# Performance work log

Hardware: AMD Instinct MI355X
Metric: run time of the kernel (lower is better)

The kernel has to match this reference:

```python
import jax, jax.numpy as jnp
import numpy as np

EPS = 1e-6

def _rms_norm(x, w):
    # RMSNorm over last dim (head_dim)
    var = jnp.mean(jnp.square(x), axis=-1, keepdims=True)
    return x * jax.lax.rsqrt(var + EPS) * w

def _apply_rope(x, cos, sin):
    # x: [b, s, h, d]; cos/sin: [s, d]. Interleaved (real, imag) pairs as in
    # diffusers apply_rotary_emb (use_real_unbind_dim=-1) used by Flux.
    xr = x[..., 0::2]
    xi = x[..., 1::2]
    rotated = jnp.stack([-xi, xr], axis=-1).reshape(x.shape)
    cs = cos[None, :, None, :]
    sn = sin[None, :, None, :]
    return x * cs + rotated * sn

def setup_inputs() -> dict:
    key = jax.random.key(0)
    ks = jax.random.split(key, 10)
    b, s, dim, h, hd = 1, 2048, 3072, 24, 128
    inner = h * hd
    scale = 1.0 / np.sqrt(dim)
    x = jax.random.normal(ks[0], (b, s, dim), dtype=jnp.float32)
    # rope tables: proper cos/sin of log-spaced frequencies
    pos = jnp.arange(s, dtype=jnp.float32)[:, None]
    freqs = 1.0 / (10000.0 ** (jnp.arange(0, hd, 2, dtype=jnp.float32) / hd))
    angles = pos * freqs[None, :]                      # [s, hd/2]
    angles = jnp.repeat(angles, 2, axis=-1)            # [s, hd] interleaved pairs
    rope_cos = jnp.cos(angles)
    rope_sin = jnp.sin(angles)
    Wq = jax.random.normal(ks[1], (dim, inner), dtype=jnp.float32) * scale
    Wk = jax.random.normal(ks[2], (dim, inner), dtype=jnp.float32) * scale
    Wv = jax.random.normal(ks[3], (dim, inner), dtype=jnp.float32) * scale
    bq = jax.random.normal(ks[4], (inner,), dtype=jnp.float32) * 0.01
    bk = jax.random.normal(ks[5], (inner,), dtype=jnp.float32) * 0.01
    bv = jax.random.normal(ks[6], (inner,), dtype=jnp.float32) * 0.01
    gq = jnp.ones((hd,), dtype=jnp.float32)
    gk = jnp.ones((hd,), dtype=jnp.float32)
    return {"x": x, "rope_cos": rope_cos, "rope_sin": rope_sin,
            "Wq": Wq, "bq": bq, "Wk": Wk, "bk": bk, "Wv": Wv, "bv": bv,
            "gq": gq, "gk": gk}

def reference(x, rope_cos, rope_sin, Wq, bq, Wk, bk, Wv, bv, gq, gk):
    b, s, _ = x.shape
    h, hd = 24, 128
    q = (x @ Wq + bq).reshape(b, s, h, hd)
    k = (x @ Wk + bk).reshape(b, s, h, hd)
    v = (x @ Wv + bv).reshape(b, s, h, hd)
    q = _apply_rope(_rms_norm(q, gq), rope_cos, rope_sin)
    k = _apply_rope(_rms_norm(k, gk), rope_cos, rope_sin)
    scale = 1.0 / jnp.sqrt(jnp.asarray(hd, dtype=q.dtype))
    scores = jnp.einsum('bshd,bthd->bhst', q, k) * scale
    attn = jax.nn.softmax(scores, axis=-1)
    out = jnp.einsum('bhst,bthd->bshd', attn, v)
    return out.reshape(b, s, h * hd)
```

## Files before the change

### kernel.cpp

```cpp
#include <hip/hip_runtime.h>
#include <hip/hip_bf16.h>

typedef __attribute__((ext_vector_type(8))) short short8;
typedef __attribute__((ext_vector_type(4))) float f32x4;
typedef __attribute__((ext_vector_type(16))) float f32x16;

#define SEQ 2048
#define DIM 3072
#define NHEAD 24
#define HDIM 128
#define SCALE_Q 0.12751744f

__device__ __forceinline__ unsigned short f2bf(float f) {
  unsigned int b = __float_as_uint(f);
  b += 0x7fffu + ((b >> 16) & 1u);
  return (unsigned short)(b >> 16);
}
__device__ __forceinline__ float bf2f(unsigned short u) {
  return __uint_as_float(((unsigned int)u) << 16);
}
__device__ __forceinline__ unsigned int pkbf(float a, float b) {
  __hip_bfloat162 h = __float22bfloat162_rn(make_float2(a, b));
  return *(unsigned int*)&h;
}

__device__ __forceinline__ void async16(const void* g, void* l) {
  __builtin_amdgcn_global_load_lds(
      (const __attribute__((address_space(1))) unsigned int*)g,
      (__attribute__((address_space(3))) unsigned int*)l, 16, 0, 0);
}

__global__ void k_cvt_x(const float* __restrict__ x, unsigned short* __restrict__ xb) {
  int idx = (blockIdx.x * 256 + threadIdx.x) * 8;
  float4 a = *(const float4*)(x + idx);
  float4 b = *(const float4*)(x + idx + 4);
  short8 o;
  o[0] = (short)f2bf(a.x); o[1] = (short)f2bf(a.y);
  o[2] = (short)f2bf(a.z); o[3] = (short)f2bf(a.w);
  o[4] = (short)f2bf(b.x); o[5] = (short)f2bf(b.y);
  o[6] = (short)f2bf(b.z); o[7] = (short)f2bf(b.w);
  *(short8*)(xb + idx) = o;
}

__device__ __forceinline__ void transpose_tile(const float* __restrict__ w,
                                               unsigned short* __restrict__ wt,
                                               int n0, int k0, int outRowBase, int t) {
  __shared__ unsigned short tile[64][68];
  int c4 = (t & 15) * 4;
  int r0 = t >> 4;
#pragma unroll
  for (int j = 0; j < 4; ++j) {
    int r = r0 + 16 * j;
    float4 v = *(const float4*)(w + (size_t)(k0 + r) * DIM + n0 + c4);
    ushort4 u;
    u.x = f2bf(v.x); u.y = f2bf(v.y); u.z = f2bf(v.z); u.w = f2bf(v.w);
    *(ushort4*)&tile[r][c4] = u;
  }
  __syncthreads();
#pragma unroll
  for (int j = 0; j < 4; ++j) {
    int nn = r0 + 16 * j;
    ushort4 u;
    u.x = tile[c4 + 0][nn]; u.y = tile[c4 + 1][nn];
    u.z = tile[c4 + 2][nn]; u.w = tile[c4 + 3][nn];
    *(ushort4*)(wt + (size_t)(outRowBase + n0 + nn) * DIM + k0 + c4) = u;
  }
}

__global__ __launch_bounds__(256) void k_transpose(const float* __restrict__ w,
                                                   unsigned short* __restrict__ wt) {
  transpose_tile(w, wt, blockIdx.x * 64, blockIdx.y * 64, 0, threadIdx.x);
}

__global__ __launch_bounds__(256) void k_transpose3(const float* __restrict__ w0,
                                                    const float* __restrict__ w1,
                                                    const float* __restrict__ w2,
                                                    unsigned short* __restrict__ wt) {
  const float* w = blockIdx.z == 0 ? w0 : (blockIdx.z == 1 ? w1 : w2);
  transpose_tile(w, wt, blockIdx.x * 64, blockIdx.y * 64, blockIdx.z * DIM, threadIdx.x);
}

__device__ __forceinline__ void gemm_tile(const unsigned short* __restrict__ xb,
                                          const unsigned short* __restrict__ wt,
                                          int bm, int bn, int t, f32x4 (&acc)[4][4],
                                          unsigned short* As, unsigned short* Bs) {
  int l = t & 63, w = t >> 6;
  int wr = w >> 1, wc = w & 1;
  int lr = l & 15, kc = l >> 4;
  const char* aB = (const char*)xb;
  const char* bB = (const char*)wt;
  char* asmB = (char*)As;
  char* bsmB = (char*)Bs;
  int sw = (lr & 7) << 4;

  for (int k0 = 0; k0 < DIM; k0 += 64) {
#pragma unroll
    for (int i = 0; i < 4; ++i) {
      int off = (t + 256 * i) * 16;
      int row = off >> 7;
      int cb = off & 127;
      int scb = cb ^ ((row & 7) << 4);
      async16(aB + ((size_t)(bm * 128 + row) * DIM + k0) * 2 + scb, asmB + off);
      async16(bB + ((size_t)(bn * 128 + row) * DIM + k0) * 2 + scb, bsmB + off);
    }
    __syncthreads();
#pragma unroll
    for (int kk = 0; kk < 2; ++kk) {
      short8 af[4], bf[4];
#pragma unroll
      for (int m = 0; m < 4; ++m)
        af[m] = *(const short8*)(asmB + (wr * 64 + m * 16 + lr) * 128 +
                                 ((kk * 64 + kc * 16) ^ sw));
#pragma unroll
      for (int n = 0; n < 4; ++n)
        bf[n] = *(const short8*)(bsmB + (wc * 64 + n * 16 + lr) * 128 +
                                 ((kk * 64 + kc * 16) ^ sw));
#pragma unroll
      for (int m = 0; m < 4; ++m)
#pragma unroll
        for (int n = 0; n < 4; ++n)
          acc[m][n] = __builtin_amdgcn_mfma_f32_16x16x32_bf16(af[m], bf[n], acc[m][n], 0, 0, 0);
    }
    __syncthreads();
  }
}

__global__ __launch_bounds__(256) void k_gemm(const unsigned short* __restrict__ xb,
                                              const unsigned short* __restrict__ wt,
                                              const float* __restrict__ bias,
                                              unsigned short* __restrict__ out,
                                              int vmode) {
  __shared__ unsigned short As[128 * 64];
  __shared__ unsigned short Bs[128 * 64];
  int t = threadIdx.x;
  int fid = blockIdx.x;
  int logical = (fid & 7) * 48 + (fid >> 3);
  int bm = logical & 15, bn = logical >> 4;

  f32x4 acc[4][4];
#pragma unroll
  for (int m = 0; m < 4; ++m)
#pragma unroll
    for (int n = 0; n < 4; ++n) acc[m][n] = (f32x4){0.f, 0.f, 0.f, 0.f};

  gemm_tile(xb, wt, bm, bn, t, acc, As, Bs);

  int l = t & 63, w = t >> 6;
  int wr = w >> 1, wc = w & 1;
  int lr = l & 15, lq = l >> 4;
  if (vmode) {
#pragma unroll
    for (int m = 0; m < 4; ++m)
#pragma unroll
      for (int n = 0; n < 4; ++n) {
        int gcol = bn * 128 + wc * 64 + n * 16 + lr;
        float bv = bias[gcol];
        int grow = bm * 128 + wr * 64 + m * 16 + lq * 4;
        ushort4 u;
        u.x = f2bf(acc[m][n][0] + bv);
        u.y = f2bf(acc[m][n][1] + bv);
        u.z = f2bf(acc[m][n][2] + bv);
        u.w = f2bf(acc[m][n][3] + bv);
        *(ushort4*)(out + (size_t)gcol * SEQ + grow) = u;
      }
  } else {
#pragma unroll
    for (int m = 0; m < 4; ++m)
#pragma unroll
      for (int n = 0; n < 4; ++n) {
        int gcol = bn * 128 + wc * 64 + n * 16 + lr;
        float bv = bias[gcol];
#pragma unroll
        for (int i = 0; i < 4; ++i) {
          int grow = bm * 128 + wr * 64 + m * 16 + lq * 4 + i;
          out[(size_t)grow * DIM + gcol] = f2bf(acc[m][n][i] + bv);
        }
      }
  }
}

__global__ __launch_bounds__(256, 4) void k_gemm3(
    const unsigned short* __restrict__ xb, const unsigned short* __restrict__ wt,
    const float* __restrict__ bq, const float* __restrict__ bk,
    const float* __restrict__ bv, const float* __restrict__ rope_cos,
    const float* __restrict__ rope_sin, const float* __restrict__ gq,
    const float* __restrict__ gk, unsigned short* __restrict__ qb,
    unsigned short* __restrict__ kb, unsigned short* __restrict__ vtb) {
  __shared__ unsigned short As[128 * 64];
  __shared__ unsigned short Bs[128 * 64];
  __shared__ float ssum[2][128];
  int t = threadIdx.x;
  int fid = blockIdx.x;
  int xcd = fid & 7, li = fid >> 3;
  int c = li / 36, r = li % 36;
  int bnl9 = r >> 2, bmi = r & 3;
  int bm = c * 4 + bmi;
  int bn = xcd * 9 + bnl9;

  f32x4 acc[4][4];
#pragma unroll
  for (int m = 0; m < 4; ++m)
#pragma unroll
    for (int n = 0; n < 4; ++n) acc[m][n] = (f32x4){0.f, 0.f, 0.f, 0.f};

  gemm_tile(xb, wt, bm, bn, t, acc, As, Bs);

  int l = t & 63, w = t >> 6;
  int wr = w >> 1, wc = w & 1;
  int lr = l & 15, lq = l >> 4;

  int region = bn >= 48 ? 2 : (bn >= 24 ? 1 : 0);
  int bnl = bn - region * 24;
  const float* bias = region == 0 ? bq : (region == 1 ? bk : bv);

  if (region == 2) {
#pragma unroll
    for (int m = 0; m < 4; ++m)
#pragma unroll
      for (int n = 0; n < 4; ++n) {
        int gcol = bnl * 128 + wc * 64 + n * 16 + lr;
        float bv_ = bias[gcol];
        int grow = bm * 128 + wr * 64 + m * 16 + lq * 4;
        ushort4 u;
        u.x = f2bf(acc[m][n][0] + bv_);
        u.y = f2bf(acc[m][n][1] + bv_);
        u.z = f2bf(acc[m][n][2] + bv_);
        u.w = f2bf(acc[m][n][3] + bv_);
        *(ushort4*)(vtb + (size_t)gcol * SEQ + grow) = u;
      }
  } else {
    unsigned short* outp = region == 0 ? qb : kb;
    const float* g = region == 0 ? gq : gk;
    float scale = region == 0 ? SCALE_Q : 1.0f;

    float gv[4], bvv[4];
#pragma unroll
    for (int n = 0; n < 4; ++n) {
      int cl = wc * 64 + n * 16 + lr;
      gv[n] = g[cl];
      bvv[n] = bias[bnl * 128 + cl];
    }
#pragma unroll
    for (int m = 0; m < 4; ++m)
#pragma unroll
      for (int n = 0; n < 4; ++n)
#pragma unroll
        for (int i = 0; i < 4; ++i) acc[m][n][i] += bvv[n];

#pragma unroll
    for (int m = 0; m < 4; ++m)
#pragma unroll
      for (int i = 0; i < 4; ++i) {
        float ss = acc[m][0][i] * acc[m][0][i] + acc[m][1][i] * acc[m][1][i] +
                   acc[m][2][i] * acc[m][2][i] + acc[m][3][i] * acc[m][3][i];
        ss += __shfl_xor(ss, 1);
        ss += __shfl_xor(ss, 2);
        ss += __shfl_xor(ss, 4);
        ss += __shfl_xor(ss, 8);
        if (lr == m * 4 + i) ssum[wc][wr * 64 + m * 16 + lq * 4 + i] = ss;
      }
    __syncthreads();

#pragma unroll
    for (int m = 0; m < 4; ++m)
#pragma unroll
      for (int i = 0; i < 4; ++i) {
        int rl = wr * 64 + m * 16 + lq * 4 + i;
        float rn = rsqrtf((ssum[0][rl] + ssum[1][rl]) * (1.0f / 128.0f) + 1e-6f);
        int s_idx = bm * 128 + rl;
        const float* cr = rope_cos + (size_t)s_idx * HDIM;
        const float* sr = rope_sin + (size_t)s_idx * HDIM;
        unsigned short* orow = outp + (size_t)s_idx * DIM + bnl * 128;
#pragma unroll
        for (int n = 0; n < 4; ++n) {
          int cl = wc * 64 + n * 16 + lr;
          float xn = acc[m][n][i] * rn * gv[n];
          float pr = __shfl_xor(xn, 1);
          float cv = cr[cl], sv = sr[cl];
          float o = (lr & 1) ? fmaf(xn, cv, pr * sv) : fmaf(xn, cv, -pr * sv);
          orow[cl] = f2bf(o * scale);
        }
      }
  }
}

__global__ void k_normrope(unsigned short* __restrict__ qk, const float* __restrict__ cosb,
                           const float* __restrict__ sinb, const float* __restrict__ g,
                           float scale) {
  int t = threadIdx.x;
  int w = t >> 6, l = t & 63;
  int row = blockIdx.x * 4 + w;
  int s_idx = row / NHEAD, head = row % NHEAD;
  size_t base = (size_t)s_idx * DIM + head * HDIM;
  unsigned int pair = *(const unsigned int*)(qk + base + 2 * l);
  float x0 = bf2f((unsigned short)(pair & 0xffffu));
  float x1 = bf2f((unsigned short)(pair >> 16));
  float ss = x0 * x0 + x1 * x1;
#pragma unroll
  for (int off = 1; off < 64; off <<= 1) ss += __shfl_xor(ss, off);
  float r = rsqrtf(ss * (1.0f / 128.0f) + 1e-6f);
  float g0 = g[2 * l], g1 = g[2 * l + 1];
  float c0 = cosb[s_idx * HDIM + 2 * l], c1 = cosb[s_idx * HDIM + 2 * l + 1];
  float s0 = sinb[s_idx * HDIM + 2 * l], s1 = sinb[s_idx * HDIM + 2 * l + 1];
  float xn0 = x0 * r * g0, xn1 = x1 * r * g1;
  float o0 = (xn0 * c0 - xn1 * s0) * scale;
  float o1 = (xn1 * c1 + xn0 * s1) * scale;
  unsigned int po = (unsigned int)f2bf(o0) | ((unsigned int)f2bf(o1) << 16);
  *(unsigned int*)(qk + base + 2 * l) = po;
}

__global__ __launch_bounds__(128, 2) void k_attn(const unsigned short* __restrict__ q,
                                                 const unsigned short* __restrict__ k,
                                                 const unsigned short* __restrict__ vt,
                                                 float* __restrict__ out) {
  __shared__ unsigned short Ksm[64 * 128];
  __shared__ unsigned short Vtsm[128 * 64];
  int t = threadIdx.x;
  int w = t >> 6, l = t & 63;
  int q32 = l & 31, hi = l >> 5;
  int hi4 = hi * 4;
  int fid = blockIdx.x;
  int logical = (fid & 7) * 96 + (fid >> 3);
  int qt = logical & 31, h = logical >> 5;
  int q0w = qt * 64 + w * 32;

  const char* kbase = (const char*)k + (size_t)h * HDIM * 2;
  const char* vbase = (const char*)vt + (size_t)h * HDIM * SEQ * 2;

  int koff[8], voff[8];
#pragma unroll
  for (int i = 0; i < 8; ++i) {
    int off = (t + 128 * i) * 16;
    int krow = off >> 8, kcb = off & 255;
    koff[i] = krow * (DIM * 2) + (kcb ^ ((krow & 15) << 4));
    int vrow = off >> 7, vcb = off & 127;
    voff[i] = vrow * (SEQ * 2) + (vcb ^ ((vrow & 7) << 4));
  }

  short8 qf[8];
  {
    const unsigned short* qrow = q + (size_t)(q0w + q32) * DIM + h * HDIM;
#pragma unroll
    for (int ks = 0; ks < 8; ++ks) qf[ks] = *(const short8*)(qrow + ks * 16 + hi * 8);
  }

  f32x16 o0 = {0.f,0.f,0.f,0.f,0.f,0.f,0.f,0.f,0.f,0.f,0.f,0.f,0.f,0.f,0.f,0.f};
  f32x16 o1 = o0, o2 = o0, o3 = o0;
  float m_ = -1e30f, lsum = 0.f;
  int ksw = (q32 & 15) << 4;
  int vsw = (q32 & 7) << 4;

  union U8 { short8 s8; unsigned int u[4]; };

  for (int kt = 0; kt < 32; ++kt) {
    const char* kt_k = kbase + (size_t)kt * (64 * DIM * 2);
    const char* kt_v = vbase + kt * 128;
#pragma unroll
    for (int i = 0; i < 8; ++i) {
      int dst = (t + 128 * i) * 16;
      async16(kt_k + koff[i], (char*)Ksm + dst);
      async16(kt_v + voff[i], (char*)Vtsm + dst);
    }
    __syncthreads();

    f32x16 st0 = {0.f,0.f,0.f,0.f,0.f,0.f,0.f,0.f,0.f,0.f,0.f,0.f,0.f,0.f,0.f,0.f};
    f32x16 st1 = st0;
    {
      const char* kr0 = (const char*)Ksm + q32 * 256;
      const char* kr1 = (const char*)Ksm + (32 + q32) * 256;
      __builtin_amdgcn_s_setprio(1);
#pragma unroll
      for (int ks = 0; ks < 8; ++ks) {
        int cb = (ks * 32 + hi * 16) ^ ksw;
        short8 kf0 = *(const short8*)(kr0 + cb);
        short8 kf1 = *(const short8*)(kr1 + cb);
        st0 = __builtin_amdgcn_mfma_f32_32x32x16_bf16(kf0, qf[ks], st0, 0, 0, 0);
        st1 = __builtin_amdgcn_mfma_f32_32x32x16_bf16(kf1, qf[ks], st1, 0, 0, 0);
      }
      __builtin_amdgcn_s_setprio(0);
    }

    float mx = fmaxf(st0[0], st1[0]);
#pragma unroll
    for (int r = 1; r < 16; ++r) mx = fmaxf(mx, fmaxf(st0[r], st1[r]));
    mx = fmaxf(mx, __shfl_xor(mx, 32));

    if (__any(mx > m_ + 10.0f)) {
      float mn = fmaxf(m_, mx);
      float corr = exp2f(m_ - mn);
      m_ = mn;
      lsum *= corr;
#pragma unroll
      for (int r = 0; r < 16; ++r) {
        float cr = __shfl(corr, (r & 3) + 8 * (r >> 2) + hi4);
        o0[r] *= cr; o1[r] *= cr; o2[r] *= cr; o3[r] *= cr;
      }
    }

#pragma unroll
    for (int r = 0; r < 16; ++r) {
      st0[r] = exp2f(st0[r] - m_);
      st1[r] = exp2f(st1[r] - m_);
    }
    {
      float sm = st0[0] + st1[0];
#pragma unroll
      for (int r = 1; r < 16; ++r) sm += st0[r] + st1[r];
      sm += __shfl_xor(sm, 32);
      lsum += sm;
    }

    U8 pa[4];
#pragma unroll
    for (int b = 0; b < 4; ++b) {
      unsigned int a0, a1, a2, a3;
      if (b < 2) {
        int r0 = (b & 1) * 8;
        a0 = pkbf(st0[r0 + 0], st0[r0 + 1]);
        a1 = pkbf(st0[r0 + 2], st0[r0 + 3]);
        a2 = pkbf(st0[r0 + 4], st0[r0 + 5]);
        a3 = pkbf(st0[r0 + 6], st0[r0 + 7]);
      } else {
        int r0 = (b & 1) * 8;
        a0 = pkbf(st1[r0 + 0], st1[r0 + 1]);
        a1 = pkbf(st1[r0 + 2], st1[r0 + 3]);
        a2 = pkbf(st1[r0 + 4], st1[r0 + 5]);
        a3 = pkbf(st1[r0 + 6], st1[r0 + 7]);
      }
      asm volatile("v_permlane32_swap_b32 %0, %1" : "+v"(a0), "+v"(a2));
      asm volatile("v_permlane32_swap_b32 %0, %1" : "+v"(a1), "+v"(a3));
      pa[b].u[0] = a0; pa[b].u[1] = a1; pa[b].u[2] = a2; pa[b].u[3] = a3;
    }

    __builtin_amdgcn_s_setprio(1);
#pragma unroll
    for (int ks = 0; ks < 4; ++ks) {
      int cb = (ks * 32 + hi * 16) ^ vsw;
      short8 vf0 = *(const short8*)((const char*)Vtsm + (0 * 32 + q32) * 128 + cb);
      short8 vf1 = *(const short8*)((const char*)Vtsm + (1 * 32 + q32) * 128 + cb);
      short8 vf2 = *(const short8*)((const char*)Vtsm + (2 * 32 + q32) * 128 + cb);
      short8 vf3 = *(const short8*)((const char*)Vtsm + (3 * 32 + q32) * 128 + cb);
      o0 = __builtin_amdgcn_mfma_f32_32x32x16_bf16(pa[ks].s8, vf0, o0, 0, 0, 0);
      o1 = __builtin_amdgcn_mfma_f32_32x32x16_bf16(pa[ks].s8, vf1, o1, 0, 0, 0);
      o2 = __builtin_amdgcn_mfma_f32_32x32x16_bf16(pa[ks].s8, vf2, o2, 0, 0, 0);
      o3 = __builtin_amdgcn_mfma_f32_32x32x16_bf16(pa[ks].s8, vf3, o3, 0, 0, 0);
    }
    __builtin_amdgcn_s_setprio(0);

    __syncthreads();
  }

  float inv = 1.0f / lsum;
#pragma unroll
  for (int r = 0; r < 16; ++r) {
    float fr = __shfl(inv, (r & 3) + 8 * (r >> 2) + hi4);
    int grow = q0w + (r & 3) + 8 * (r >> 2) + hi4;
    float* orow = out + (size_t)grow * DIM + h * HDIM + q32;
    orow[0]  = o0[r] * fr;
    orow[32] = o1[r] * fr;
    orow[64] = o2[r] * fr;
    orow[96] = o3[r] * fr;
  }
}

extern "C" void kernel_launch(void* const* d_in, const int* in_sizes, int n_in,
                              void* d_out, int out_size, void* d_ws, size_t ws_size,
                              hipStream_t stream) {
  const float* x = (const float*)d_in[0];
  const float* rope_cos = (const float*)d_in[1];
  const float* rope_sin = (const float*)d_in[2];
  const float* Wq = (const float*)d_in[3];
  const float* bq = (const float*)d_in[4];
  const float* Wk = (const float*)d_in[5];
  const float* bk = (const float*)d_in[6];
  const float* Wv = (const float*)d_in[7];
  const float* bv = (const float*)d_in[8];
  const float* gq = (const float*)d_in[9];
  const float* gk = (const float*)d_in[10];
  float* out = (float*)d_out;

  const size_t slab = (size_t)SEQ * DIM;
  const size_t wt9elems = (size_t)3 * DIM * DIM;
  const size_t need = (4 * slab + wt9elems) * 2;

  if (ws_size >= need) {
    unsigned short* xb = (unsigned short*)d_ws;
    unsigned short* wt9 = xb + slab;
    unsigned short* qb = wt9 + wt9elems;
    unsigned short* kb = qb + slab;
    unsigned short* vtb = kb + slab;

    k_cvt_x<<<3072, 256, 0, stream>>>(x, xb);
    k_transpose3<<<dim3(DIM / 64, DIM / 64, 3), 256, 0, stream>>>(Wq, Wk, Wv, wt9);
    k_gemm3<<<1152, 256, 0, stream>>>(xb, wt9, bq, bk, bv, rope_cos, rope_sin, gq, gk,
                                      qb, kb, vtb);
    k_attn<<<768, 128, 0, stream>>>(qb, kb, vtb, out);
  } else {
    unsigned short* xb = (unsigned short*)d_ws;
    unsigned short* wt = xb + slab;
    unsigned short* qb = wt + (size_t)DIM * DIM;
    unsigned short* kb = qb + slab;
    unsigned short* vtb = kb + slab;

    k_cvt_x<<<3072, 256, 0, stream>>>(x, xb);
    dim3 tg(DIM / 64, DIM / 64);
    k_transpose<<<tg, 256, 0, stream>>>(Wq, wt);
    k_gemm<<<384, 256, 0, stream>>>(xb, wt, bq, qb, 0);
    k_transpose<<<tg, 256, 0, stream>>>(Wk, wt);
    k_gemm<<<384, 256, 0, stream>>>(xb, wt, bk, kb, 0);
    k_transpose<<<tg, 256, 0, stream>>>(Wv, wt);
    k_gemm<<<384, 256, 0, stream>>>(xb, wt, bv, vtb, 1);
    k_normrope<<<SEQ * NHEAD / 4, 256, 0, stream>>>(qb, rope_cos, rope_sin, gq, SCALE_Q);
    k_normrope<<<SEQ * NHEAD / 4, 256, 0, stream>>>(kb, rope_cos, rope_sin, gk, 1.0f);
    k_attn<<<768, 128, 0, stream>>>(qb, kb, vtb, out);
  }
}
```

Before: 286.8 us.

## Enlarge fused QKV GEMM tile to 256x128 with inline MFMA loop

```diff
diff --git a/kernel.cpp b/kernel.cpp
--- a/kernel.cpp
+++ b/kernel.cpp
@@ -179,48 +179,90 @@
   }
 }
 
-__global__ __launch_bounds__(256, 4) void k_gemm3(
+__global__ __launch_bounds__(256, 2) void k_gemm3(
     const unsigned short* __restrict__ xb, const unsigned short* __restrict__ wt,
     const float* __restrict__ bq, const float* __restrict__ bk,
     const float* __restrict__ bv, const float* __restrict__ rope_cos,
     const float* __restrict__ rope_sin, const float* __restrict__ gq,
     const float* __restrict__ gk, unsigned short* __restrict__ qb,
     unsigned short* __restrict__ kb, unsigned short* __restrict__ vtb) {
-  __shared__ unsigned short As[128 * 64];
+  __shared__ unsigned short As[256 * 64];
   __shared__ unsigned short Bs[128 * 64];
-  __shared__ float ssum[2][128];
+  __shared__ float ssum[2][256];
   int t = threadIdx.x;
   int fid = blockIdx.x;
   int xcd = fid & 7, li = fid >> 3;
-  int c = li / 36, r = li % 36;
-  int bnl9 = r >> 2, bmi = r & 3;
-  int bm = c * 4 + bmi;
+  int c = li / 18, r = li % 18;
+  int bnl9 = r >> 1, bmi = r & 1;
+  int bm = c * 2 + bmi;
   int bn = xcd * 9 + bnl9;
-
-  f32x4 acc[4][4];
-#pragma unroll
-  for (int m = 0; m < 4; ++m)
-#pragma unroll
-    for (int n = 0; n < 4; ++n) acc[m][n] = (f32x4){0.f, 0.f, 0.f, 0.f};
-
-  gemm_tile(xb, wt, bm, bn, t, acc, As, Bs);
 
   int l = t & 63, w = t >> 6;
   int wr = w >> 1, wc = w & 1;
-  int lr = l & 15, lq = l >> 4;
-
+  int lr = l & 15, kc = l >> 4;
+  int sw = (lr & 7) << 4;
+
+  f32x4 acc[8][4];
+#pragma unroll
+  for (int m = 0; m < 8; ++m)
+#pragma unroll
+    for (int n = 0; n < 4; ++n) acc[m][n] = (f32x4){0.f, 0.f, 0.f, 0.f};
+
+  const char* aB = (const char*)xb;
+  const char* bB = (const char*)wt;
+  char* asmB = (char*)As;
+  char* bsmB = (char*)Bs;
+
+  for (int k0 = 0; k0 < DIM; k0 += 64) {
+#pragma unroll
+    for (int i = 0; i < 8; ++i) {
+      int off = (t + 256 * i) * 16;
+      int row = off >> 7;
+      int cb = off & 127;
+      int scb = cb ^ ((row & 7) << 4);
+      async16(aB + ((size_t)(bm * 256 + row) * DIM + k0) * 2 + scb, asmB + off);
+    }
+#pragma unroll
+    for (int i = 0; i < 4; ++i) {
+      int off = (t + 256 * i) * 16;
+      int row = off >> 7;
+      int cb = off & 127;
+      int scb = cb ^ ((row & 7) << 4);
+      async16(bB + ((size_t)(bn * 128 + row) * DIM + k0) * 2 + scb, bsmB + off);
+    }
+    __syncthreads();
+#pragma unroll
+    for (int kk = 0; kk < 2; ++kk) {
+      short8 af[8], bf[4];
+      int kb_ = (kk * 64 + kc * 16) ^ sw;
+#pragma unroll
+      for (int m = 0; m < 8; ++m)
+        af[m] = *(const short8*)(asmB + (wr * 128 + m * 16 + lr) * 128 + kb_);
+#pragma unroll
+      for (int n = 0; n < 4; ++n)
+        bf[n] = *(const short8*)(bsmB + (wc * 64 + n * 16 + lr) * 128 + kb_);
+#pragma unroll
+      for (int m = 0; m < 8; ++m)
+#pragma unroll
+        for (int n = 0; n < 4; ++n)
+          acc[m][n] = __builtin_amdgcn_mfma_f32_16x16x32_bf16(af[m], bf[n], acc[m][n], 0, 0, 0);
+    }
+    __syncthreads();
+  }
+
+  int lq = l >> 4;
   int region = bn >= 48 ? 2 : (bn >= 24 ? 1 : 0);
   int bnl = bn - region * 24;
   const float* bias = region == 0 ? bq : (region == 1 ? bk : bv);
 
   if (region == 2) {
 #pragma unroll
-    for (int m = 0; m < 4; ++m)
+    for (int m = 0; m < 8; ++m)
 #pragma unroll
       for (int n = 0; n < 4; ++n) {
         int gcol = bnl * 128 + wc * 64 + n * 16 + lr;
         float bv_ = bias[gcol];
-        int grow = bm * 128 + wr * 64 + m * 16 + lq * 4;
+        int grow = bm * 256 + wr * 128 + m * 16 + lq * 4;
         ushort4 u;
         u.x = f2bf(acc[m][n][0] + bv_);
         u.y = f2bf(acc[m][n][1] + bv_);
@@ -241,14 +283,14 @@
       bvv[n] = bias[bnl * 128 + cl];
     }
 #pragma unroll
-    for (int m = 0; m < 4; ++m)
+    for (int m = 0; m < 8; ++m)
 #pragma unroll
       for (int n = 0; n < 4; ++n)
 #pragma unroll
         for (int i = 0; i < 4; ++i) acc[m][n][i] += bvv[n];
 
 #pragma unroll
-    for (int m = 0; m < 4; ++m)
+    for (int m = 0; m < 8; ++m)
 #pragma unroll
       for (int i = 0; i < 4; ++i) {
         float ss = acc[m][0][i] * acc[m][0][i] + acc[m][1][i] * acc[m][1][i] +
@@ -257,17 +299,17 @@
         ss += __shfl_xor(ss, 2);
         ss += __shfl_xor(ss, 4);
         ss += __shfl_xor(ss, 8);
-        if (lr == m * 4 + i) ssum[wc][wr * 64 + m * 16 + lq * 4 + i] = ss;
-      }
-    __syncthreads();
-
-#pragma unroll
-    for (int m = 0; m < 4; ++m)
+        if (lr == ((m * 4 + i) & 15)) ssum[wc][wr * 128 + m * 16 + lq * 4 + i] = ss;
+      }
+    __syncthreads();
+
+#pragma unroll
+    for (int m = 0; m < 8; ++m)
 #pragma unroll
       for (int i = 0; i < 4; ++i) {
-        int rl = wr * 64 + m * 16 + lq * 4 + i;
+        int rl = wr * 128 + m * 16 + lq * 4 + i;
         float rn = rsqrtf((ssum[0][rl] + ssum[1][rl]) * (1.0f / 128.0f) + 1e-6f);
-        int s_idx = bm * 128 + rl;
+        int s_idx = bm * 256 + rl;
         const float* cr = rope_cos + (size_t)s_idx * HDIM;
         const float* sr = rope_sin + (size_t)s_idx * HDIM;
         unsigned short* orow = outp + (size_t)s_idx * DIM + bnl * 128;
@@ -492,8 +534,8 @@
 
     k_cvt_x<<<3072, 256, 0, stream>>>(x, xb);
     k_transpose3<<<dim3(DIM / 64, DIM / 64, 3), 256, 0, stream>>>(Wq, Wk, Wv, wt9);
-    k_gemm3<<<1152, 256, 0, stream>>>(xb, wt9, bq, bk, bv, rope_cos, rope_sin, gq, gk,
-                                      qb, kb, vtb);
+    k_gemm3<<<576, 256, 0, stream>>>(xb, wt9, bq, bk, bv, rope_cos, rope_sin, gq, gk,
+                                     qb, kb, vtb);
     k_attn<<<768, 128, 0, stream>>>(qb, kb, vtb, out);
   } else {
     unsigned short* xb = (unsigned short*)d_ws;
```

Measured after the change: 312.3 us. 8.9% more time.

## Split KV loop across two wave pairs per block and merge softmax partials

Applied to the files above, without the earlier changes.

```diff
diff --git a/kernel.cpp b/kernel.cpp
--- a/kernel.cpp
+++ b/kernel.cpp
@@ -309,28 +309,30 @@
   *(unsigned int*)(qk + base + 2 * l) = po;
 }
 
-__global__ __launch_bounds__(128, 2) void k_attn(const unsigned short* __restrict__ q,
+__global__ __launch_bounds__(256, 2) void k_attn(const unsigned short* __restrict__ q,
                                                  const unsigned short* __restrict__ k,
                                                  const unsigned short* __restrict__ vt,
                                                  float* __restrict__ out) {
-  __shared__ unsigned short Ksm[64 * 128];
-  __shared__ unsigned short Vtsm[128 * 64];
+  __shared__ unsigned short Ksm[2][64 * 128];
+  __shared__ unsigned short Vtsm[2][128 * 64];
   int t = threadIdx.x;
   int w = t >> 6, l = t & 63;
+  int qhalf = w & 1, par = w >> 1;
   int q32 = l & 31, hi = l >> 5;
   int hi4 = hi * 4;
   int fid = blockIdx.x;
   int logical = (fid & 7) * 96 + (fid >> 3);
   int qt = logical & 31, h = logical >> 5;
-  int q0w = qt * 64 + w * 32;
+  int q0w = qt * 64 + qhalf * 32;
 
   const char* kbase = (const char*)k + (size_t)h * HDIM * 2;
   const char* vbase = (const char*)vt + (size_t)h * HDIM * SEQ * 2;
 
-  int koff[8], voff[8];
-#pragma unroll
-  for (int i = 0; i < 8; ++i) {
-    int off = (t + 128 * i) * 16;
+  int koff[4], voff[4], dst[4];
+#pragma unroll
+  for (int i = 0; i < 4; ++i) {
+    int off = (t + 256 * i) * 16;
+    dst[i] = off;
     int krow = off >> 8, kcb = off & 255;
     koff[i] = krow * (DIM * 2) + (kcb ^ ((krow & 15) << 4));
     int vrow = off >> 7, vcb = off & 127;
@@ -352,22 +354,25 @@
 
   union U8 { short8 s8; unsigned int u[4]; };
 
-  for (int kt = 0; kt < 32; ++kt) {
-    const char* kt_k = kbase + (size_t)kt * (64 * DIM * 2);
-    const char* kt_v = vbase + kt * 128;
-#pragma unroll
-    for (int i = 0; i < 8; ++i) {
-      int dst = (t + 128 * i) * 16;
-      async16(kt_k + koff[i], (char*)Ksm + dst);
-      async16(kt_v + voff[i], (char*)Vtsm + dst);
+  for (int t2 = 0; t2 < 16; ++t2) {
+    int kt0 = t2 * 2;
+#pragma unroll
+    for (int p = 0; p < 2; ++p) {
+      const char* kt_k = kbase + (size_t)(kt0 + p) * (64 * DIM * 2);
+      const char* kt_v = vbase + (kt0 + p) * 128;
+#pragma unroll
+      for (int i = 0; i < 4; ++i) {
+        async16(kt_k + koff[i], (char*)Ksm[p] + dst[i]);
+        async16(kt_v + voff[i], (char*)Vtsm[p] + dst[i]);
+      }
     }
     __syncthreads();
 
     f32x16 st0 = {0.f,0.f,0.f,0.f,0.f,0.f,0.f,0.f,0.f,0.f,0.f,0.f,0.f,0.f,0.f,0.f};
     f32x16 st1 = st0;
     {
-      const char* kr0 = (const char*)Ksm + q32 * 256;
-      const char* kr1 = (const char*)Ksm + (32 + q32) * 256;
+      const char* kr0 = (const char*)Ksm[par] + q32 * 256;
+      const char* kr1 = (const char*)Ksm[par] + (32 + q32) * 256;
       __builtin_amdgcn_s_setprio(1);
 #pragma unroll
       for (int ks = 0; ks < 8; ++ks) {
@@ -436,10 +441,11 @@
 #pragma unroll
     for (int ks = 0; ks < 4; ++ks) {
       int cb = (ks * 32 + hi * 16) ^ vsw;
-      short8 vf0 = *(const short8*)((const char*)Vtsm + (0 * 32 + q32) * 128 + cb);
-      short8 vf1 = *(const short8*)((const char*)Vtsm + (1 * 32 + q32) * 128 + cb);
-      short8 vf2 = *(const short8*)((const char*)Vtsm + (2 * 32 + q32) * 128 + cb);
-      short8 vf3 = *(const short8*)((const char*)Vtsm + (3 * 32 + q32) * 128 + cb);
+      const char* Vp = (const char*)Vtsm[par];
+      short8 vf0 = *(const short8*)(Vp + (0 * 32 + q32) * 128 + cb);
+      short8 vf1 = *(const short8*)(Vp + (1 * 32 + q32) * 128 + cb);
+      short8 vf2 = *(const short8*)(Vp + (2 * 32 + q32) * 128 + cb);
+      short8 vf3 = *(const short8*)(Vp + (3 * 32 + q32) * 128 + cb);
       o0 = __builtin_amdgcn_mfma_f32_32x32x16_bf16(pa[ks].s8, vf0, o0, 0, 0, 0);
       o1 = __builtin_amdgcn_mfma_f32_32x32x16_bf16(pa[ks].s8, vf1, o1, 0, 0, 0);
       o2 = __builtin_amdgcn_mfma_f32_32x32x16_bf16(pa[ks].s8, vf2, o2, 0, 0, 0);
@@ -450,16 +456,40 @@
     __syncthreads();
   }
 
-  float inv = 1.0f / lsum;
-#pragma unroll
-  for (int r = 0; r < 16; ++r) {
-    float fr = __shfl(inv, (r & 3) + 8 * (r >> 2) + hi4);
-    int grow = q0w + (r & 3) + 8 * (r >> 2) + hi4;
-    float* orow = out + (size_t)grow * DIM + h * HDIM + q32;
-    orow[0]  = o0[r] * fr;
-    orow[32] = o1[r] * fr;
-    orow[64] = o2[r] * fr;
-    orow[96] = o3[r] * fr;
+  float* mbase = (float*)(&Ksm[0][0]) + qhalf * 4224;
+  float* oB = mbase;
+  float* mB = mbase + 4096;
+  float* lB = mbase + 4128;
+  if (par == 1) {
+#pragma unroll
+    for (int r = 0; r < 16; ++r) {
+      oB[r * 64 + l]        = o0[r];
+      oB[(16 + r) * 64 + l] = o1[r];
+      oB[(32 + r) * 64 + l] = o2[r];
+      oB[(48 + r) * 64 + l] = o3[r];
+    }
+    if (l < 32) { mB[l] = m_; lB[l] = lsum; }
+  }
+  __syncthreads();
+  if (par == 0) {
+    float mBv = mB[q32];
+    float lBv = lB[q32];
+    float mN = fmaxf(m_, mBv);
+    float cA = exp2f(m_ - mN), cB = exp2f(mBv - mN);
+    float inv = 1.0f / (lsum * cA + lBv * cB);
+    float fA = cA * inv, fB = cB * inv;
+#pragma unroll
+    for (int r = 0; r < 16; ++r) {
+      int crow = (r & 3) + 8 * (r >> 2) + hi4;
+      float sA = __shfl(fA, crow);
+      float sB = __shfl(fB, crow);
+      int grow = q0w + crow;
+      float* orow = out + (size_t)grow * DIM + h * HDIM + q32;
+      orow[0]  = o0[r] * sA + oB[r * 64 + l] * sB;
+      orow[32] = o1[r] * sA + oB[(16 + r) * 64 + l] * sB;
+      orow[64] = o2[r] * sA + oB[(32 + r) * 64 + l] * sB;
+      orow[96] = o3[r] * sA + oB[(48 + r) * 64 + l] * sB;
+    }
   }
 }
 
@@ -494,7 +524,7 @@
     k_transpose3<<<dim3(DIM / 64, DIM / 64, 3), 256, 0, stream>>>(Wq, Wk, Wv, wt9);
     k_gemm3<<<1152, 256, 0, stream>>>(xb, wt9, bq, bk, bv, rope_cos, rope_sin, gq, gk,
                                       qb, kb, vtb);
-    k_attn<<<768, 128, 0, stream>>>(qb, kb, vtb, out);
+    k_attn<<<768, 256, 0, stream>>>(qb, kb, vtb, out);
   } else {
     unsigned short* xb = (unsigned short*)d_ws;
     unsigned short* wt = xb + slab;
@@ -512,6 +542,6 @@
     k_gemm<<<384, 256, 0, stream>>>(xb, wt, bv, vtb, 1);
     k_normrope<<<SEQ * NHEAD / 4, 256, 0, stream>>>(qb, rope_cos, rope_sin, gq, SCALE_Q);
     k_normrope<<<SEQ * NHEAD / 4, 256, 0, stream>>>(kb, rope_cos, rope_sin, gk, 1.0f);
-    k_attn<<<768, 128, 0, stream>>>(qb, kb, vtb, out);
-  }
-}
+    k_attn<<<768, 256, 0, stream>>>(qb, kb, vtb, out);
+  }
+}
```

Measured after the change: 285.2 us. About the same (-0.6%).

## Double-buffer K/V tiles in attention and widen blocks to four waves

Applied to the files above, without the earlier changes.

```diff
diff --git a/kernel.cpp b/kernel.cpp
--- a/kernel.cpp
+++ b/kernel.cpp
@@ -309,28 +309,29 @@
   *(unsigned int*)(qk + base + 2 * l) = po;
 }
 
-__global__ __launch_bounds__(128, 2) void k_attn(const unsigned short* __restrict__ q,
+__global__ __launch_bounds__(256, 2) void k_attn(const unsigned short* __restrict__ q,
                                                  const unsigned short* __restrict__ k,
                                                  const unsigned short* __restrict__ vt,
                                                  float* __restrict__ out) {
-  __shared__ unsigned short Ksm[64 * 128];
-  __shared__ unsigned short Vtsm[128 * 64];
+  __shared__ unsigned short Ksm[2][64 * 128];
+  __shared__ unsigned short Vtsm[2][128 * 64];
   int t = threadIdx.x;
   int w = t >> 6, l = t & 63;
   int q32 = l & 31, hi = l >> 5;
   int hi4 = hi * 4;
   int fid = blockIdx.x;
-  int logical = (fid & 7) * 96 + (fid >> 3);
-  int qt = logical & 31, h = logical >> 5;
-  int q0w = qt * 64 + w * 32;
+  int logical = (fid & 7) * 48 + (fid >> 3);
+  int qt = logical & 15, h = logical >> 4;
+  int q0w = qt * 128 + w * 32;
 
   const char* kbase = (const char*)k + (size_t)h * HDIM * 2;
   const char* vbase = (const char*)vt + (size_t)h * HDIM * SEQ * 2;
 
-  int koff[8], voff[8];
-#pragma unroll
-  for (int i = 0; i < 8; ++i) {
-    int off = (t + 128 * i) * 16;
+  int koff[4], voff[4], dst[4];
+#pragma unroll
+  for (int i = 0; i < 4; ++i) {
+    int off = (t + 256 * i) * 16;
+    dst[i] = off;
     int krow = off >> 8, kcb = off & 255;
     koff[i] = krow * (DIM * 2) + (kcb ^ ((krow & 15) << 4));
     int vrow = off >> 7, vcb = off & 127;
@@ -352,22 +353,30 @@
 
   union U8 { short8 s8; unsigned int u[4]; };
 
+#pragma unroll
+  for (int i = 0; i < 4; ++i) {
+    async16(kbase + koff[i], (char*)Ksm[0] + dst[i]);
+    async16(vbase + voff[i], (char*)Vtsm[0] + dst[i]);
+  }
+  __syncthreads();
+
   for (int kt = 0; kt < 32; ++kt) {
-    const char* kt_k = kbase + (size_t)kt * (64 * DIM * 2);
-    const char* kt_v = vbase + kt * 128;
-#pragma unroll
-    for (int i = 0; i < 8; ++i) {
-      int dst = (t + 128 * i) * 16;
-      async16(kt_k + koff[i], (char*)Ksm + dst);
-      async16(kt_v + voff[i], (char*)Vtsm + dst);
-    }
-    __syncthreads();
+    int cur = kt & 1;
+    if (kt < 31) {
+      const char* kt_k = kbase + (size_t)(kt + 1) * (64 * DIM * 2);
+      const char* kt_v = vbase + (kt + 1) * 128;
+#pragma unroll
+      for (int i = 0; i < 4; ++i) {
+        async16(kt_k + koff[i], (char*)Ksm[cur ^ 1] + dst[i]);
+        async16(kt_v + voff[i], (char*)Vtsm[cur ^ 1] + dst[i]);
+      }
+    }
 
     f32x16 st0 = {0.f,0.f,0.f,0.f,0.f,0.f,0.f,0.f,0.f,0.f,0.f,0.f,0.f,0.f,0.f,0.f};
     f32x16 st1 = st0;
     {
-      const char* kr0 = (const char*)Ksm + q32 * 256;
-      const char* kr1 = (const char*)Ksm + (32 + q32) * 256;
+      const char* kr0 = (const char*)Ksm[cur] + q32 * 256;
+      const char* kr1 = (const char*)Ksm[cur] + (32 + q32) * 256;
       __builtin_amdgcn_s_setprio(1);
 #pragma unroll
       for (int ks = 0; ks < 8; ++ks) {
@@ -436,10 +445,11 @@
 #pragma unroll
     for (int ks = 0; ks < 4; ++ks) {
       int cb = (ks * 32 + hi * 16) ^ vsw;
-      short8 vf0 = *(const short8*)((const char*)Vtsm + (0 * 32 + q32) * 128 + cb);
-      short8 vf1 = *(const short8*)((const char*)Vtsm + (1 * 32 + q32) * 128 + cb);
-      short8 vf2 = *(const short8*)((const char*)Vtsm + (2 * 32 + q32) * 128 + cb);
-      short8 vf3 = *(const short8*)((const char*)Vtsm + (3 * 32 + q32) * 128 + cb);
+      const char* Vp = (const char*)Vtsm[cur];
+      short8 vf0 = *(const short8*)(Vp + (0 * 32 + q32) * 128 + cb);
+      short8 vf1 = *(const short8*)(Vp + (1 * 32 + q32) * 128 + cb);
+      short8 vf2 = *(const short8*)(Vp + (2 * 32 + q32) * 128 + cb);
+      short8 vf3 = *(const short8*)(Vp + (3 * 32 + q32) * 128 + cb);
       o0 = __builtin_amdgcn_mfma_f32_32x32x16_bf16(pa[ks].s8, vf0, o0, 0, 0, 0);
       o1 = __builtin_amdgcn_mfma_f32_32x32x16_bf16(pa[ks].s8, vf1, o1, 0, 0, 0);
       o2 = __builtin_amdgcn_mfma_f32_32x32x16_bf16(pa[ks].s8, vf2, o2, 0, 0, 0);
@@ -494,7 +504,7 @@
     k_transpose3<<<dim3(DIM / 64, DIM / 64, 3), 256, 0, stream>>>(Wq, Wk, Wv, wt9);
     k_gemm3<<<1152, 256, 0, stream>>>(xb, wt9, bq, bk, bv, rope_cos, rope_sin, gq, gk,
                                       qb, kb, vtb);
-    k_attn<<<768, 128, 0, stream>>>(qb, kb, vtb, out);
+    k_attn<<<384, 256, 0, stream>>>(qb, kb, vtb, out);
   } else {
     unsigned short* xb = (unsigned short*)d_ws;
     unsigned short* wt = xb + slab;
@@ -512,6 +522,6 @@
     k_gemm<<<384, 256, 0, stream>>>(xb, wt, bv, vtb, 1);
     k_normrope<<<SEQ * NHEAD / 4, 256, 0, stream>>>(qb, rope_cos, rope_sin, gq, SCALE_Q);
     k_normrope<<<SEQ * NHEAD / 4, 256, 0, stream>>>(kb, rope_cos, rope_sin, gk, 1.0f);
-    k_attn<<<768, 128, 0, stream>>>(qb, kb, vtb, out);
-  }
-}
+    k_attn<<<384, 256, 0, stream>>>(qb, kb, vtb, out);
+  }
+}
```

Measured after the change: 282.1 us. Within noise of the previous version (-1.6%).
